# Optimization experiments

Hardware: AMD Instinct MI355X
Metric: run time of the kernel (lower is better)

## Reference

```python
import jax, jax.numpy as jnp
import numpy as np

IMAGE_SIZE = 224
COV_HP = 1.0
SIGMA = 1.0
STEPS = 2
CUTOFF = 20.0
IMP_LO, IMP_HI = 0.5, 2.0
REL_W = 0.5
EPS = 1e-6

# Projection matrices for front/top/left views (buffer Js in the module)
JS = jnp.array([[[1, 0, 0], [0, 1, 0]],
                [[1, 0, 0], [0, 0, 1]],
                [[0, 0, 1], [0, 1, 0]]], dtype=jnp.float32)


def _blur(d, sigma):
    # d: [B,H,W]; separable Gaussian blur, 'same' padding
    r = max(1, int(3 * sigma))
    x = jnp.arange(-r, r + 1, dtype=jnp.float32)
    k = jnp.exp(-(x * x) / (2.0 * sigma * sigma))
    k = k / k.sum()
    d4 = d[:, None]  # [B,1,H,W]
    kh = k.reshape(1, 1, -1, 1)
    kw = k.reshape(1, 1, 1, -1)
    d4 = jax.lax.conv_general_dilated(d4, kh, (1, 1), [(r, r), (0, 0)],
                                      dimension_numbers=('NCHW', 'OIHW', 'NCHW'))
    d4 = jax.lax.conv_general_dilated(d4, kw, (1, 1), [(0, 0), (r, r)],
                                      dimension_numbers=('NCHW', 'OIHW', 'NCHW'))
    return d4[:, 0]


def _fill_depth_map(d, sigma, steps):
    # fill_depth_map is not defined in the source; implemented as iterative
    # Gaussian-blur hole filling (empty pixels take blurred neighborhood).
    for _ in range(steps):
        b = _blur(d, sigma)
        d = jnp.where(d > 1e-6, d, b)
    return d


def _forward(position, cov3d, opacity, importance):
    B, N, _ = position.shape
    H = W = IMAGE_SIZE
    Hh, Wh = H // 2, W // 2
    yy, xx = jnp.meshgrid(jnp.arange(Hh), jnp.arange(Wh), indexing='ij')
    grid = jnp.stack([xx, yy], axis=-1).astype(jnp.float32)  # [Hh,Wh,2]
    imp = jnp.clip(jnp.broadcast_to(importance[:, :N], (B, N)), IMP_LO, IMP_HI)
    imp = imp[:, :, None, None]
    eye3 = jnp.eye(3, dtype=cov3d.dtype)
    eye2 = jnp.eye(2, dtype=cov3d.dtype)
    maps = []
    for v in range(3):  # fixed small view loop, as in the source
        J = JS[v]  # [2,3]
        # NOTE: source mutates cov3d across the view loop; replicate that
        cov3d = (cov3d + jnp.swapaxes(cov3d, -1, -2)) * 0.5
        cov3d = cov3d + EPS * eye3
        nrm = jnp.linalg.norm(cov3d, axis=(-1, -2), keepdims=True)
        cov3d = cov3d / (nrm + EPS) * COV_HP
        cinv = jnp.linalg.inv(cov3d)                               # [B,N,3,3]
        cov2d_inv = jnp.einsum('ij,bnjk,lk->bnil', J, cinv, J)     # J C^-1 J^T
        cov2d_inv = cov2d_inv + eye2 * (EPS * 1e-4)
        proj = jnp.einsum('bnk,jk->bnj', position, J)              # [B,N,2]
        mn = proj.min(axis=1, keepdims=True)
        mx = proj.max(axis=1, keepdims=True)
        rng = mx - mn + 1e-6
        mn = mn - 0.5 * rng
        mx = mx + 0.5 * rng
        rng = mx - mn + 1e-6
        xy = jnp.clip((proj - mn) / rng * (Wh - 1), 0.0, Wh - 1)
        delta = grid[None, None] - xy[:, :, None, None, :]         # [B,N,Hh,Wh,2]
        mask_h = jnp.linalg.norm(delta, axis=-1) < CUTOFF
        mask = jnp.repeat(jnp.repeat(mask_h, 2, axis=2), 2, axis=3)
        exph = -jnp.einsum('bnhwj,bnjk,bnhwk->bnhw', delta, cov2d_inv, delta)
        exp_full = jax.image.resize(exph, (B, N, H, W), method='bilinear')
        exp_full = jnp.clip(exp_full, -20.0, 0.0)
        w = opacity[:, :, None, None] * imp * jnp.exp(exp_full)
        w = jnp.where(mask, w, 0.0)
        wmin = w.min(axis=1, keepdims=True)
        wmax = w.max(axis=1, keepdims=True)
        nw = (w - wmin) / (wmax - wmin + EPS) * REL_W + w / (w.sum(axis=1, keepdims=True) + EPS)
        dm = nw.sum(axis=1)  # [B,H,W]
        maps.append(_fill_depth_map(dm, SIGMA, STEPS))
    d = jnp.stack(maps, axis=1)  # [B,3,H,W], already 224x224 so resize is a no-op
    d = (d - d.mean()) / (jnp.std(d, ddof=1) + EPS)
    return d


def setup_inputs() -> dict:
    key = jax.random.key(0)
    k1, k2, k3 = jax.random.split(key, 3)
    B, N, MAXG = 1, 512, 1000
    return {
        'position': jax.random.normal(k1, (B, N, 3), dtype=jnp.float32),
        'cov3d': jax.random.normal(k2, (B, N, 3, 3), dtype=jnp.float32),
        'opacity': jax.random.uniform(k3, (B, N), dtype=jnp.float32),
        'importance': jnp.ones((1, MAXG), dtype=jnp.float32),
    }


def reference(position, cov3d, opacity, importance):
    return _forward(position, cov3d, opacity, importance)
```

## Files before the change

kernel.cpp:

```cpp
#include <hip/hip_runtime.h>
#include <math.h>


__device__ __forceinline__ float wave_min(float v) {
    #pragma unroll
    for (int o = 32; o >= 1; o >>= 1) v = fminf(v, __shfl_xor(v, o));
    return v;
}

__global__ __launch_bounds__(512) void splat_fused_kernel(
    const float* __restrict__ position, const float* __restrict__ cov3d,
    const float* __restrict__ opacity, const float* __restrict__ importance,
    float* __restrict__ dm) {
    __shared__ float4 lsA[512];
    __shared__ float2 lsB[512];
    __shared__ float red[8 * 6];
    __shared__ float pS[7][64], pMn[7][64], pMx[7][64];
    __shared__ int cnt;
    const int v = blockIdx.z;
    const int tx0 = blockIdx.x * 8, ty0 = blockIdx.y * 8;
    const int tid = threadIdx.x;
    const int lane = tid & 63, wave = tid >> 6;

    const int n = tid;
    const float p0 = position[n * 3 + 0];
    const float p1 = position[n * 3 + 1];
    const float p2 = position[n * 3 + 2];
    const float opimp = opacity[n] * fminf(fmaxf(importance[n], 0.5f), 2.0f);

    {
        float vals[6] = {p0, -p0, p1, -p1, p2, -p2};
        #pragma unroll
        for (int k = 0; k < 6; ++k) {
            float r = wave_min(vals[k]);
            if (lane == 0) red[wave * 6 + k] = r;
        }
    }
    __syncthreads();
    float mn6[6];
    #pragma unroll
    for (int k = 0; k < 6; ++k) {
        float r = red[k];
        #pragma unroll
        for (int w = 1; w < 8; ++w) r = fminf(r, red[w * 6 + k]);
        mn6[k] = r;
    }
    const float pmn[3] = {mn6[0], mn6[2], mn6[4]};
    const float pmx[3] = {-mn6[1], -mn6[3], -mn6[5]};

    float c00 = cov3d[n * 9 + 0], c01 = cov3d[n * 9 + 1], c02 = cov3d[n * 9 + 2];
    float c10 = cov3d[n * 9 + 3], c11 = cov3d[n * 9 + 4], c12 = cov3d[n * 9 + 5];
    float c20 = cov3d[n * 9 + 6], c21 = cov3d[n * 9 + 7], c22 = cov3d[n * 9 + 8];
    for (int vv = 0; vv <= v; ++vv) {
        float s01 = 0.5f * (c01 + c10);
        float s02 = 0.5f * (c02 + c20);
        float s12 = 0.5f * (c12 + c21);
        float s00 = c00 + 1e-6f;
        float s11 = c11 + 1e-6f;
        float s22 = c22 + 1e-6f;
        float nrm = sqrtf(s00 * s00 + s11 * s11 + s22 * s22 +
                          2.0f * (s01 * s01 + s02 * s02 + s12 * s12));
        float inv = 1.0f / (nrm + 1e-6f);
        c00 = s00 * inv; c11 = s11 * inv; c22 = s22 * inv;
        c01 = s01 * inv; c10 = c01; c02 = s02 * inv; c20 = c02;
        c12 = s12 * inv; c21 = c12;
    }
    float cof00 = c11 * c22 - c12 * c12;
    float cof01 = c02 * c12 - c01 * c22;
    float cof02 = c01 * c12 - c02 * c11;
    float det = c00 * cof00 + c01 * cof01 + c02 * cof02;
    float idet = 1.0f / det;
    float i00 = cof00 * idet;
    float i01 = cof01 * idet;
    float i02 = cof02 * idet;
    float i11 = (c00 * c22 - c02 * c02) * idet;
    float i12 = (c02 * c01 - c00 * c12) * idet;
    float i22 = (c00 * c11 - c01 * c01) * idet;

    float Aa, Ab, Ac, prx, pry;
    int ix, iy;
    if (v == 0)      { Aa = i00; Ab = i01; Ac = i11; prx = p0; pry = p1; ix = 0; iy = 1; }
    else if (v == 1) { Aa = i00; Ab = i02; Ac = i22; prx = p0; pry = p2; ix = 0; iy = 2; }
    else             { Aa = i22; Ab = i12; Ac = i11; prx = p2; pry = p1; ix = 2; iy = 1; }
    Aa += 1e-10f;
    Ac += 1e-10f;

    float mnx = pmn[ix], mxx = pmx[ix], mny = pmn[iy], mxy = pmx[iy];
    float rngx = mxx - mnx + 1e-6f;
    float mnx2 = mnx - 0.5f * rngx;
    float mxx2 = mxx + 0.5f * rngx;
    rngx = mxx2 - mnx2 + 1e-6f;
    float rngy = mxy - mny + 1e-6f;
    float mny2 = mny - 0.5f * rngy;
    float mxy2 = mxy + 0.5f * rngy;
    rngy = mxy2 - mny2 + 1e-6f;
    float gx = fminf(fmaxf((prx - mnx2) / rngx * 111.0f, 0.0f), 111.0f);
    float gy = fminf(fmaxf((pry - mny2) / rngy * 111.0f, 0.0f), 111.0f);

    if (tid == 0) cnt = 0;
    __syncthreads();
    {
        const float bx0 = (float)(tx0 >> 1), bx1 = (float)((tx0 + 7) >> 1);
        const float by0 = (float)(ty0 >> 1), by1 = (float)((ty0 + 7) >> 1);
        float dx = fmaxf(fmaxf(bx0 - gx, gx - bx1), 0.0f);
        float dy = fmaxf(fmaxf(by0 - gy, gy - by1), 0.0f);
        bool pass = (dx * dx + dy * dy) < 400.01f;
        unsigned long long m = __ballot(pass);
        int base = 0;
        if (lane == 0) base = atomicAdd(&cnt, __popcll(m));
        base = __shfl(base, 0);
        if (pass) {
            int slot = base + __popcll(m & ((1ull << lane) - 1ull));
            lsA[slot] = make_float4(Aa, 2.0f * Ab, Ac, opimp);
            lsB[slot] = make_float2(gx, gy);
        }
    }
    __syncthreads();
    const int len = cnt;

    const int rep = wave;
    const int xo = tx0 + (lane & 7);
    const int yo = ty0 + (lane >> 3);

    if (len == 0) {
        if (rep == 0) dm[(v * 224 + yo) * 224 + xo] = 0.0f;
        return;
    }

    const int npad = (len + 31) & ~31;
    if (tid < npad - len) {
        lsA[len + tid] = make_float4(1.0f, 0.0f, 1.0f, 0.0f);
        lsB[len + tid] = make_float2(1e9f, 1e9f);
    }
    __syncthreads();

    const int xh = xo >> 1, yh = yo >> 1;
    const int px = xo & 1, py = yo & 1;
    int xlo = xh - 1 + px; int xhi = min(xlo + 1, 111); xlo = max(xlo, 0);
    int ylo = yh - 1 + py; int yhi = min(ylo + 1, 111); ylo = max(ylo, 0);
    const float wxlo = px ? 0.75f : 0.25f, wxhi = 1.0f - wxlo;
    const float wylo = py ? 0.75f : 0.25f, wyhi = 1.0f - wylo;
    const float fx0 = (float)xlo, fx1 = (float)xhi;
    const float fy0 = (float)ylo, fy1 = (float)yhi;
    const float ex = wxlo * fx0 + wxhi * fx1;
    const float ey = wylo * fy0 + wyhi * fy1;
    const float Vx = wxlo * wxhi * (fx1 - fx0) * (fx1 - fx0);
    const float Vy = wylo * wyhi * (fy1 - fy0) * (fy1 - fy0);
    const float fxh = (float)xh, fyh = (float)yh;

    float S = 0.0f, wmn = INFINITY, wmx = -INFINITY;
    for (int base = rep * 4; base < npad; base += 32) {
        float4 ga[4];
        float2 gb[4];
        #pragma unroll
        for (int k = 0; k < 4; ++k) {
            ga[k] = lsA[base + k];
            gb[k] = lsB[base + k];
        }
        #pragma unroll
        for (int k = 0; k < 4; ++k) {
            const float xx = gb[k].x, yy = gb[k].y;
            const float dxh = fxh - xx, dyh = fyh - yy;
            const bool m = dxh * dxh + dyh * dyh < 400.0f;
            const float dx = ex - xx, dy = ey - yy;
            float q = dx * (ga[k].x * dx + ga[k].y * dy) + ga[k].z * dy * dy;
            float bil = -(q + ga[k].x * Vx + ga[k].z * Vy);
            bil = fminf(fmaxf(bil, -20.0f), 0.0f);
            bil = m ? bil : -1e9f;
            float w = ga[k].w * __expf(bil);
            S += w; wmn = fminf(wmn, w); wmx = fmaxf(wmx, w);
        }
    }
    if (rep > 0) { pS[rep - 1][lane] = S; pMn[rep - 1][lane] = wmn; pMx[rep - 1][lane] = wmx; }
    __syncthreads();
    if (rep == 0) {
        #pragma unroll
        for (int k = 0; k < 7; ++k) {
            S += pS[k][lane];
            wmn = fminf(wmn, pMn[k][lane]);
            wmx = fmaxf(wmx, pMx[k][lane]);
        }
        if (len < 512) { wmn = fminf(wmn, 0.0f); wmx = fmaxf(wmx, 0.0f); }
        float dmv = 0.5f * (S - 512.0f * wmn) / (wmx - wmn + 1e-6f) + S / (S + 1e-6f);
        dm[(v * 224 + yo) * 224 + xo] = dmv;
    }
}

__global__ __launch_bounds__(256) void blur2_stats_kernel(
    const float* __restrict__ in, float* __restrict__ out,
    float2* __restrict__ partials) {
    __shared__ float A[28 * 29];
    __shared__ float T[28 * 29];
    __shared__ float r1[4], r2[4];
    const int v = blockIdx.z;
    const int tx0 = blockIdx.x * 16, ty0 = blockIdx.y * 16;
    const int tid = threadIdx.x;
    const float kw[7] = {0.00443305f, 0.05400558f, 0.24203623f, 0.39905030f,
                         0.24203623f, 0.05400558f, 0.00443305f};
    const float* __restrict__ chan = in + v * 224 * 224;

    for (int idx = tid; idx < 28 * 28; idx += 256) {
        int rr = idx / 28, c = idx % 28;
        int gyy = ty0 - 6 + rr, gxx = tx0 - 6 + c;
        float val = 0.0f;
        if (gyy >= 0 && gyy < 224 && gxx >= 0 && gxx < 224) val = chan[gyy * 224 + gxx];
        A[rr * 29 + c] = val;
    }
    __syncthreads();
    for (int idx = tid; idx < 22 * 28; idx += 256) {
        int rr = 3 + idx / 28, c = idx % 28;
        float s = 0.0f;
        #pragma unroll
        for (int i = 0; i < 7; ++i) s += kw[i] * A[(rr - 3 + i) * 29 + c];
        T[rr * 29 + c] = s;
    }
    __syncthreads();
    for (int idx = tid; idx < 22 * 22; idx += 256) {
        int rr = 3 + idx / 22, c = 3 + idx % 22;
        int gyy = ty0 - 6 + rr, gxx = tx0 - 6 + c;
        float s = 0.0f;
        #pragma unroll
        for (int j = 0; j < 7; ++j) s += kw[j] * T[rr * 29 + c - 3 + j];
        float ctr = A[rr * 29 + c];
        float d1 = ctr > 1e-6f ? ctr : s;
        if (gyy < 0 || gyy > 223 || gxx < 0 || gxx > 223) d1 = 0.0f;
        A[rr * 29 + c] = d1;
    }
    __syncthreads();
    for (int idx = tid; idx < 16 * 22; idx += 256) {
        int rr = 6 + idx / 22, c = 3 + idx % 22;
        float s = 0.0f;
        #pragma unroll
        for (int i = 0; i < 7; ++i) s += kw[i] * A[(rr - 3 + i) * 29 + c];
        T[rr * 29 + c] = s;
    }
    __syncthreads();
    float ls1 = 0.0f, ls2 = 0.0f;
    for (int idx = tid; idx < 16 * 16; idx += 256) {
        int rr = 6 + (idx >> 4), c = 6 + (idx & 15);
        float s = 0.0f;
        #pragma unroll
        for (int j = 0; j < 7; ++j) s += kw[j] * T[rr * 29 + c - 3 + j];
        float ctr = A[rr * 29 + c];
        float d2 = ctr > 1e-6f ? ctr : s;
        out[(v * 224 + ty0 + rr - 6) * 224 + (tx0 + c - 6)] = d2;
        ls1 += d2; ls2 += d2 * d2;
    }
    #pragma unroll
    for (int o = 32; o >= 1; o >>= 1) {
        ls1 += __shfl_xor(ls1, o);
        ls2 += __shfl_xor(ls2, o);
    }
    if ((tid & 63) == 0) { r1[tid >> 6] = ls1; r2[tid >> 6] = ls2; }
    __syncthreads();
    if (tid == 0) {
        float s1 = r1[0] + r1[1] + r1[2] + r1[3];
        float s2 = r2[0] + r2[1] + r2[2] + r2[3];
        partials[(blockIdx.z * 14 + blockIdx.y) * 14 + blockIdx.x] = make_float2(s1, s2);
    }
}

__global__ __launch_bounds__(256) void normalize_kernel(
    const float2* __restrict__ partials, float* __restrict__ out) {
    __shared__ double s1[256], s2[256];
    const int tid = threadIdx.x;
    double a = 0.0, b = 0.0;
    for (int i = tid; i < 588; i += 256) {
        float2 p = partials[i];
        a += (double)p.x; b += (double)p.y;
    }
    s1[tid] = a; s2[tid] = b;
    __syncthreads();
    for (int s = 128; s >= 1; s >>= 1) {
        if (tid < s) { s1[tid] += s1[tid + s]; s2[tid] += s2[tid + s]; }
        __syncthreads();
    }
    const double M = 150528.0;
    double mean = s1[0] / M;
    double var = (s2[0] - M * mean * mean) / (M - 1.0);
    double sd = sqrt(var > 0.0 ? var : 0.0);
    const int idx = blockIdx.x * 256 + tid;
    if (idx < 3 * 224 * 224)
        out[idx] = (out[idx] - (float)mean) / ((float)sd + 1e-6f);
}

extern "C" void kernel_launch(void* const* d_in, const int* in_sizes, int n_in,
                              void* d_out, int out_size, void* d_ws, size_t ws_size,
                              hipStream_t stream) {
    const float* position   = (const float*)d_in[0];
    const float* cov3d      = (const float*)d_in[1];
    const float* opacity    = (const float*)d_in[2];
    const float* importance = (const float*)d_in[3];
    float* out = (float*)d_out;

    float* dmA       = (float*)d_ws;
    float2* partials = (float2*)((float*)d_ws + 150528);

    hipLaunchKernelGGL(splat_fused_kernel, dim3(28, 28, 3), dim3(512), 0, stream,
                       position, cov3d, opacity, importance, dmA);
    hipLaunchKernelGGL(blur2_stats_kernel, dim3(14, 14, 3), dim3(256), 0, stream,
                       dmA, out, partials);
    hipLaunchKernelGGL(normalize_kernel, dim3(588), dim3(256), 0, stream,
                       partials, out);
}
```

Baseline: 95.07 us.

## Compute 2x2 output pixels per lane sharing half-res Gaussian terms, 16x16 tiles

Each lane now owns one half-resolution grid cell and evaluates the four full-resolution pixels that map to it. The per-Gaussian inside test and the partial quadratic terms are shared across those four pixels. Tiles grow from 8x8 to 16x16 pixels, so the grid shrinks fourfold and the per-block setup (position min/max reduction, culling, compaction) is amortised over more output. The risk is that the wider tile culls fewer Gaussians per block, and 588 blocks may underfill the GPU. Register pressure and shared-memory partials also rise with the float4 accumulators.

```diff
diff --git a/kernel.cpp b/kernel.cpp
--- a/kernel.cpp
+++ b/kernel.cpp
@@ -15,10 +15,10 @@
     __shared__ float4 lsA[512];
     __shared__ float2 lsB[512];
     __shared__ float red[8 * 6];
-    __shared__ float pS[7][64], pMn[7][64], pMx[7][64];
+    __shared__ float4 pS[7][64], pMn[7][64], pMx[7][64];
     __shared__ int cnt;
     const int v = blockIdx.z;
-    const int tx0 = blockIdx.x * 8, ty0 = blockIdx.y * 8;
+    const int tx0 = blockIdx.x * 16, ty0 = blockIdx.y * 16;
     const int tid = threadIdx.x;
     const int lane = tid & 63, wave = tid >> 6;
 
@@ -100,8 +100,8 @@
     if (tid == 0) cnt = 0;
     __syncthreads();
     {
-        const float bx0 = (float)(tx0 >> 1), bx1 = (float)((tx0 + 7) >> 1);
-        const float by0 = (float)(ty0 >> 1), by1 = (float)((ty0 + 7) >> 1);
+        const float bx0 = (float)(tx0 >> 1), bx1 = (float)((tx0 + 15) >> 1);
+        const float by0 = (float)(ty0 >> 1), by1 = (float)((ty0 + 15) >> 1);
         float dx = fmaxf(fmaxf(bx0 - gx, gx - bx1), 0.0f);
         float dy = fmaxf(fmaxf(by0 - gy, gy - by1), 0.0f);
         bool pass = (dx * dx + dy * dy) < 400.01f;
@@ -118,71 +118,123 @@
     __syncthreads();
     const int len = cnt;
 
-    const int rep = wave;
-    const int xo = tx0 + (lane & 7);
-    const int yo = ty0 + (lane >> 3);
+    const int qx = lane & 7, qy = lane >> 3;
+    const int xh = (tx0 >> 1) + qx;
+    const int yh = (ty0 >> 1) + qy;
 
     if (len == 0) {
-        if (rep == 0) dm[(v * 224 + yo) * 224 + xo] = 0.0f;
+        if (wave == 0) {
+            #pragma unroll
+            for (int py = 0; py < 2; ++py)
+                #pragma unroll
+                for (int px = 0; px < 2; ++px)
+                    dm[(v * 224 + ty0 + 2 * qy + py) * 224 + tx0 + 2 * qx + px] = 0.0f;
+        }
         return;
     }
 
-    const int npad = (len + 31) & ~31;
+    const int npad = (len + 15) & ~15;
     if (tid < npad - len) {
         lsA[len + tid] = make_float4(1.0f, 0.0f, 1.0f, 0.0f);
         lsB[len + tid] = make_float2(1e9f, 1e9f);
     }
     __syncthreads();
 
-    const int xh = xo >> 1, yh = yo >> 1;
-    const int px = xo & 1, py = yo & 1;
-    int xlo = xh - 1 + px; int xhi = min(xlo + 1, 111); xlo = max(xlo, 0);
-    int ylo = yh - 1 + py; int yhi = min(ylo + 1, 111); ylo = max(ylo, 0);
-    const float wxlo = px ? 0.75f : 0.25f, wxhi = 1.0f - wxlo;
-    const float wylo = py ? 0.75f : 0.25f, wyhi = 1.0f - wylo;
-    const float fx0 = (float)xlo, fx1 = (float)xhi;
-    const float fy0 = (float)ylo, fy1 = (float)yhi;
-    const float ex = wxlo * fx0 + wxhi * fx1;
-    const float ey = wylo * fy0 + wyhi * fy1;
-    const float Vx = wxlo * wxhi * (fx1 - fx0) * (fx1 - fx0);
-    const float Vy = wylo * wyhi * (fy1 - fy0) * (fy1 - fy0);
+    float exA[2], eyA[2], VxA[2], VyA[2];
+    #pragma unroll
+    for (int p = 0; p < 2; ++p) {
+        int xlo = xh - 1 + p; int xhi = min(xlo + 1, 111); xlo = max(xlo, 0);
+        float wlo = p ? 0.75f : 0.25f, whi = 1.0f - wlo;
+        exA[p] = wlo * (float)xlo + whi * (float)xhi;
+        VxA[p] = wlo * whi * (float)(xhi - xlo) * (float)(xhi - xlo);
+        int ylo = yh - 1 + p; int yhi2 = min(ylo + 1, 111); ylo = max(ylo, 0);
+        eyA[p] = wlo * (float)ylo + whi * (float)yhi2;
+        VyA[p] = wlo * whi * (float)(yhi2 - ylo) * (float)(yhi2 - ylo);
+    }
     const float fxh = (float)xh, fyh = (float)yh;
 
-    float S = 0.0f, wmn = INFINITY, wmx = -INFINITY;
-    for (int base = rep * 4; base < npad; base += 32) {
-        float4 ga[4];
-        float2 gb[4];
-        #pragma unroll
-        for (int k = 0; k < 4; ++k) {
-            ga[k] = lsA[base + k];
-            gb[k] = lsB[base + k];
-        }
-        #pragma unroll
-        for (int k = 0; k < 4; ++k) {
-            const float xx = gb[k].x, yy = gb[k].y;
+    const int chunk = npad >> 3;
+    const int cbeg = wave * chunk, cend = cbeg + chunk;
+
+    float S00 = 0.f, S01 = 0.f, S10 = 0.f, S11 = 0.f;
+    float mn00 = INFINITY, mn01 = INFINITY, mn10 = INFINITY, mn11 = INFINITY;
+    float mx00 = -INFINITY, mx01 = -INFINITY, mx10 = -INFINITY, mx11 = -INFINITY;
+
+    for (int i = cbeg; i < cend; i += 2) {
+        float4 gA0 = lsA[i], gA1 = lsA[i + 1];
+        float2 gB0 = lsB[i], gB1 = lsB[i + 1];
+        #pragma unroll
+        for (int u = 0; u < 2; ++u) {
+            const float4 gA = u ? gA1 : gA0;
+            const float2 gB = u ? gB1 : gB0;
+            const float a = gA.x, b2 = gA.y, c = gA.z, op = gA.w;
+            const float xx = gB.x, yy = gB.y;
             const float dxh = fxh - xx, dyh = fyh - yy;
-            const bool m = dxh * dxh + dyh * dyh < 400.0f;
-            const float dx = ex - xx, dy = ey - yy;
-            float q = dx * (ga[k].x * dx + ga[k].y * dy) + ga[k].z * dy * dy;
-            float bil = -(q + ga[k].x * Vx + ga[k].z * Vy);
-            bil = fminf(fmaxf(bil, -20.0f), 0.0f);
-            bil = m ? bil : -1e9f;
-            float w = ga[k].w * __expf(bil);
-            S += w; wmn = fminf(wmn, w); wmx = fmaxf(wmx, w);
-        }
-    }
-    if (rep > 0) { pS[rep - 1][lane] = S; pMn[rep - 1][lane] = wmn; pMx[rep - 1][lane] = wmx; }
-    __syncthreads();
-    if (rep == 0) {
+            const bool inside = dxh * dxh + dyh * dyh < 400.0f;
+            const float dx0 = exA[0] - xx, dx1 = exA[1] - xx;
+            const float dy0 = eyA[0] - yy, dy1 = eyA[1] - yy;
+            const float adx0 = a * dx0, adx1 = a * dx1;
+            const float bdy0 = b2 * dy0, bdy1 = b2 * dy1;
+            const float cdy0 = c * dy0 * dy0, cdy1 = c * dy1 * dy1;
+            const float ax0 = a * VxA[0], ax1 = a * VxA[1];
+            const float cy0 = c * VyA[0], cy1 = c * VyA[1];
+            #pragma unroll
+            for (int py = 0; py < 2; ++py) {
+                const float dyp  = py ? dy1 : dy0;
+                const float bdyp = py ? bdy1 : bdy0;
+                const float cdyp = py ? cdy1 : cdy0;
+                const float cyp  = py ? cy1 : cy0;
+                #pragma unroll
+                for (int px = 0; px < 2; ++px) {
+                    const float dxp  = px ? dx1 : dx0;
+                    const float adxp = px ? adx1 : adx0;
+                    const float axp  = px ? ax1 : ax0;
+                    float q = dxp * (adxp + bdyp) + cdyp;
+                    float bil = -((q + axp) + cyp);
+                    bil = fminf(fmaxf(bil, -20.0f), 0.0f);
+                    bil = inside ? bil : -1e9f;
+                    float w = op * __expf(bil);
+                    if (py == 0 && px == 0) { S00 += w; mn00 = fminf(mn00, w); mx00 = fmaxf(mx00, w); }
+                    if (py == 0 && px == 1) { S01 += w; mn01 = fminf(mn01, w); mx01 = fmaxf(mx01, w); }
+                    if (py == 1 && px == 0) { S10 += w; mn10 = fminf(mn10, w); mx10 = fmaxf(mx10, w); }
+                    if (py == 1 && px == 1) { S11 += w; mn11 = fminf(mn11, w); mx11 = fmaxf(mx11, w); }
+                }
+            }
+        }
+    }
+    if (wave > 0) {
+        pS[wave - 1][lane]  = make_float4(S00, S01, S10, S11);
+        pMn[wave - 1][lane] = make_float4(mn00, mn01, mn10, mn11);
+        pMx[wave - 1][lane] = make_float4(mx00, mx01, mx10, mx11);
+    }
+    __syncthreads();
+    if (wave == 0) {
         #pragma unroll
         for (int k = 0; k < 7; ++k) {
-            S += pS[k][lane];
-            wmn = fminf(wmn, pMn[k][lane]);
-            wmx = fmaxf(wmx, pMx[k][lane]);
-        }
-        if (len < 512) { wmn = fminf(wmn, 0.0f); wmx = fmaxf(wmx, 0.0f); }
-        float dmv = 0.5f * (S - 512.0f * wmn) / (wmx - wmn + 1e-6f) + S / (S + 1e-6f);
-        dm[(v * 224 + yo) * 224 + xo] = dmv;
+            float4 s = pS[k][lane], m = pMn[k][lane], M = pMx[k][lane];
+            S00 += s.x; S01 += s.y; S10 += s.z; S11 += s.w;
+            mn00 = fminf(mn00, m.x); mn01 = fminf(mn01, m.y);
+            mn10 = fminf(mn10, m.z); mn11 = fminf(mn11, m.w);
+            mx00 = fmaxf(mx00, M.x); mx01 = fmaxf(mx01, M.y);
+            mx10 = fmaxf(mx10, M.z); mx11 = fmaxf(mx11, M.w);
+        }
+        if (len < 512) {
+            mn00 = fminf(mn00, 0.f); mn01 = fminf(mn01, 0.f);
+            mn10 = fminf(mn10, 0.f); mn11 = fminf(mn11, 0.f);
+            mx00 = fmaxf(mx00, 0.f); mx01 = fmaxf(mx01, 0.f);
+            mx10 = fmaxf(mx10, 0.f); mx11 = fmaxf(mx11, 0.f);
+        }
+        float S4[4]  = {S00, S01, S10, S11};
+        float mn4[4] = {mn00, mn01, mn10, mn11};
+        float mx4[4] = {mx00, mx01, mx10, mx11};
+        #pragma unroll
+        for (int pp = 0; pp < 4; ++pp) {
+            float S = S4[pp];
+            float dmv = 0.5f * (S - 512.0f * mn4[pp]) / (mx4[pp] - mn4[pp] + 1e-6f)
+                      + S / (S + 1e-6f);
+            const int py = pp >> 1, px = pp & 1;
+            dm[(v * 224 + ty0 + 2 * qy + py) * 224 + tx0 + 2 * qx + px] = dmv;
+        }
     }
 }
 
@@ -296,7 +348,7 @@
     float* dmA       = (float*)d_ws;
     float2* partials = (float2*)((float*)d_ws + 150528);
 
-    hipLaunchKernelGGL(splat_fused_kernel, dim3(28, 28, 3), dim3(512), 0, stream,
+    hipLaunchKernelGGL(splat_fused_kernel, dim3(14, 14, 3), dim3(512), 0, stream,
                        position, cov3d, opacity, importance, dmA);
     hipLaunchKernelGGL(blur2_stats_kernel, dim3(14, 14, 3), dim3(256), 0, stream,
                        dmA, out, partials);
```

Result: faster. 89.80 us (-5.5%).
